# Kernel tuning notes

Hardware: AMD Instinct MI355X
Metric: run time of the kernel (lower is better)

Reference implementation:

```python
import jax, jax.numpy as jnp
import numpy as np
from itertools import permutations

B, S, D = 1024, 16, 128
G_DIMS = [256, 256]
F_DIMS = [256, 256]

# all ordered pairs (i, j), i != j, in the same lexicographic order as
# itertools.permutations used by the torch module
_PAIRS = np.array(list(permutations(range(S), 2)), dtype=np.int32)  # [P, 2], P = S*(S-1)


def _init_linear(key, in_dim, out_dim):
    kw, kb = jax.random.split(key)
    bound = 1.0 / np.sqrt(in_dim)
    W = jax.random.uniform(kw, (in_dim, out_dim), jnp.float32, -bound, bound)
    b = jax.random.uniform(kb, (out_dim,), jnp.float32, -bound, bound)
    return W, b


def setup_inputs() -> dict:
    key = jax.random.key(0)
    ks = jax.random.split(key, 5)
    state = jax.random.normal(ks[0], (B, S, D), jnp.float32)
    gW0, gb0 = _init_linear(ks[1], 2 * D, G_DIMS[0])
    gW1, gb1 = _init_linear(ks[2], G_DIMS[0], G_DIMS[1])
    fW0, fb0 = _init_linear(ks[3], G_DIMS[1], F_DIMS[0])
    fW1, fb1 = _init_linear(ks[4], F_DIMS[0], F_DIMS[1])
    return {"state": state,
            "gW0": gW0, "gb0": gb0, "gW1": gW1, "gb1": gb1,
            "fW0": fW0, "fb0": fb0, "fW1": fW1, "fb1": fb1}


def reference(state, gW0, gb0, gW1, gb1, fW0, fb0, fW1, fb1):
    i_idx = jnp.asarray(_PAIRS[:, 0])
    j_idx = jnp.asarray(_PAIRS[:, 1])
    # gather + concat all ordered pairs: [B, P, 2D]
    paired = jnp.concatenate([state[:, i_idx], state[:, j_idx]], axis=-1)
    # g-MLP applied per pair
    h = jax.nn.relu(jnp.einsum('bpd,de->bpe', paired, gW0) + gb0)
    h = jax.nn.relu(jnp.einsum('bpd,de->bpe', h, gW1) + gb1)
    # sum over pairs -> [B, g_out]
    pooled = h.sum(axis=1)
    # f-MLP
    out = jax.nn.relu(pooled @ fW0 + fb0)
    out = jax.nn.relu(out @ fW1 + fb1)
    return out
```

## Files before the change

### kernel.cpp

```cpp
#include <hip/hip_runtime.h>

typedef __attribute__((ext_vector_type(8))) _Float16 f16x8;
typedef __attribute__((ext_vector_type(4))) float f32x4;

#define HSTR 264

__global__ __launch_bounds__(256) void prep_kernel(
    const float* __restrict__ gW0, const float* __restrict__ gW1,
    _Float16* __restrict__ W0c, _Float16* __restrict__ W1c)
{
  const int t = blockIdx.x * 256 + threadIdx.x;
  {
    const int c = t >> 7, k = t & 127;
    const int dst = ((k >> 5) * 32 + (c >> 4)) * 512 +
                    (((k >> 3) & 3) * 16 + (c & 15)) * 8 + (k & 7);
    const int src = (k + ((c >= 256) ? 128 : 0)) * 256 + (c & 255);
    W0c[dst] = (_Float16)gW0[src];
  }
  {
    const int n = t >> 8, k = t & 255;
    const int dst = ((k >> 5) * 16 + (n >> 4)) * 512 +
                    (((k >> 3) & 3) * 16 + (n & 15)) * 8 + (k & 7);
    W1c[dst] = (_Float16)gW1[k * 256 + n];
  }
}

__global__ __launch_bounds__(512, 4) void pair_kernel(
    const float* __restrict__ state,
    const _Float16* __restrict__ W0c, const float* __restrict__ gb0,
    const _Float16* __restrict__ W1c, const float* __restrict__ gb1,
    float* __restrict__ pooled)
{
  const int b   = blockIdx.x;
  const int tid = threadIdx.x;
  const int w   = tid >> 6;
  const int l   = tid & 63;
  const int lr  = l & 15;
  const int lg  = l >> 4;

  __shared__ _Float16 A_lds[16 * HSTR];
  __shared__ _Float16 C_lds[16 * HSTR];

  const float* stb = state + (size_t)b * 2048;

  f16x8 sfrag[4];
  #pragma unroll
  for (int kk = 0; kk < 4; ++kk) {
    const float* sp = stb + lr * 128 + kk * 32 + lg * 8;
    f32x4 s0 = *(const f32x4*)sp;
    f32x4 s1 = *(const f32x4*)(sp + 4);
    f16x8 f;
    f[0] = (_Float16)s0[0]; f[1] = (_Float16)s0[1];
    f[2] = (_Float16)s0[2]; f[3] = (_Float16)s0[3];
    f[4] = (_Float16)s1[0]; f[5] = (_Float16)s1[1];
    f[6] = (_Float16)s1[2]; f[7] = (_Float16)s1[3];
    sfrag[kk] = f;
  }

  const f32x4 z4 = {0.f, 0.f, 0.f, 0.f};
  f32x4 acc2[4];
  #pragma unroll
  for (int nt = 0; nt < 4; ++nt) acc2[nt] = z4;

  #pragma unroll
  for (int nt = 0; nt < 4; ++nt) {
    #pragma unroll
    for (int kk = 0; kk < 4; ++kk) {
      f16x8 bf = *(const f16x8*)(W0c + (size_t)((kk * 32 + 4 * w + nt) * 512 + l * 8));
      acc2[nt] = __builtin_amdgcn_mfma_f32_16x16x32_f16(sfrag[kk], bf, acc2[nt], 0, 0, 0);
    }
  }

  f16x8 bw[2][8];
  #pragma unroll
  for (int nt = 0; nt < 2; ++nt) {
    #pragma unroll
    for (int kk = 0; kk < 8; ++kk) {
      bw[nt][kk] = *(const f16x8*)(W1c + (size_t)((kk * 16 + 2 * w + nt) * 512 + l * 8));
      asm volatile("" : "+a"(bw[nt][kk]));
    }
  }
  float gb1v[2];
  gb1v[0] = gb1[32 * w + lr];
  gb1v[1] = gb1[32 * w + 16 + lr];

  #pragma unroll
  for (int nt = 0; nt < 4; ++nt) {
    const int col = 64 * w + 16 * nt + lr;
    #pragma unroll
    for (int r = 0; r < 4; ++r) {
      const int row = lg * 4 + r;
      const float v = acc2[nt][r];
      if (col < 256) A_lds[row * HSTR + col]       = (_Float16)(v + gb0[col]);
      else           C_lds[row * HSTR + col - 256] = (_Float16)v;
    }
  }
  __syncthreads();

  f16x8 creg[8];
  #pragma unroll
  for (int kk = 0; kk < 8; ++kk)
    creg[kk] = *(const f16x8*)&C_lds[lr * HSTR + kk * 32 + lg * 8];

  const f16x8 zh = {(_Float16)0, (_Float16)0, (_Float16)0, (_Float16)0,
                    (_Float16)0, (_Float16)0, (_Float16)0, (_Float16)0};

  float pp0 = 0.f, pp1 = 0.f;
  #pragma unroll 1
  for (int i = 0; i < 16; ++i) {
    f32x4 a0 = z4, a1 = z4;
    #pragma unroll
    for (int kk = 0; kk < 8; ++kk) {
      f16x8 av = *(const f16x8*)&A_lds[i * HSTR + kk * 32 + lg * 8];
      f16x8 u = __builtin_elementwise_max(av + creg[kk], zh);
      a0 = __builtin_amdgcn_mfma_f32_16x16x32_f16(u, bw[0][kk], a0, 0, 0, 0);
      a1 = __builtin_amdgcn_mfma_f32_16x16x32_f16(u, bw[1][kk], a1, 0, 0, 0);
    }
    #pragma unroll
    for (int r = 0; r < 4; ++r) {
      const int row = lg * 4 + r;
      const float v0 = fmaxf(a0[r] + gb1v[0], 0.f);
      const float v1 = fmaxf(a1[r] + gb1v[1], 0.f);
      pp0 += (row == i) ? 0.f : v0;
      pp1 += (row == i) ? 0.f : v1;
    }
  }

  {
    float v = pp0;
    v += __shfl_xor(v, 16);
    v += __shfl_xor(v, 32);
    if (lg == 0) pooled[(size_t)b * 256 + 32 * w + lr] = v;
  }
  {
    float v = pp1;
    v += __shfl_xor(v, 16);
    v += __shfl_xor(v, 32);
    if (lg == 0) pooled[(size_t)b * 256 + 32 * w + 16 + lr] = v;
  }
}

__global__ __launch_bounds__(256) void fmlp_kernel(
    const float* __restrict__ pooled,
    const float* __restrict__ fW0, const float* __restrict__ fb0,
    const float* __restrict__ fW1, const float* __restrict__ fb1,
    float* __restrict__ out)
{
  const int tid = threadIdx.x;
  const size_t b0 = (size_t)blockIdx.x * 4;
  __shared__ float pl[4][256];
  __shared__ float h1[4][256];

  #pragma unroll
  for (int q = 0; q < 4; ++q)
    pl[q][tid] = pooled[(b0 + q) * 256 + tid];
  __syncthreads();

  float acc[4] = {0.f, 0.f, 0.f, 0.f};
  #pragma unroll 8
  for (int k = 0; k < 256; ++k) {
    const float wv = fW0[(size_t)k * 256 + tid];
    #pragma unroll
    for (int q = 0; q < 4; ++q) acc[q] = fmaf(pl[q][k], wv, acc[q]);
  }
  #pragma unroll
  for (int q = 0; q < 4; ++q) h1[q][tid] = fmaxf(acc[q] + fb0[tid], 0.f);
  __syncthreads();

  float acc2[4] = {0.f, 0.f, 0.f, 0.f};
  #pragma unroll 8
  for (int k = 0; k < 256; ++k) {
    const float wv = fW1[(size_t)k * 256 + tid];
    #pragma unroll
    for (int q = 0; q < 4; ++q) acc2[q] = fmaf(h1[q][k], wv, acc2[q]);
  }
  #pragma unroll
  for (int q = 0; q < 4; ++q)
    out[(b0 + q) * 256 + tid] = fmaxf(acc2[q] + fb1[tid], 0.f);
}

extern "C" void kernel_launch(void* const* d_in, const int* in_sizes, int n_in,
                              void* d_out, int out_size, void* d_ws, size_t ws_size,
                              hipStream_t stream) {
  const float* state = (const float*)d_in[0];
  const float* gW0   = (const float*)d_in[1];
  const float* gb0   = (const float*)d_in[2];
  const float* gW1   = (const float*)d_in[3];
  const float* gb1   = (const float*)d_in[4];
  const float* fW0   = (const float*)d_in[5];
  const float* fb0   = (const float*)d_in[6];
  const float* fW1   = (const float*)d_in[7];
  const float* fb1   = (const float*)d_in[8];
  float* out = (float*)d_out;

  _Float16* W0c = (_Float16*)d_ws;
  _Float16* W1c = W0c + 65536;
  float* pooled = (float*)(W1c + 65536);

  const int Bn = in_sizes[0] / 2048;

  prep_kernel<<<dim3(256), dim3(256), 0, stream>>>(gW0, gW1, W0c, W1c);
  pair_kernel<<<dim3(Bn), dim3(512), 0, stream>>>(state, W0c, gb0, W1c, gb1, pooled);
  fmlp_kernel<<<dim3(Bn / 4), dim3(256), 0, stream>>>(pooled, fW0, fb0, fW1, fb1, out);
}
```

Measured before the change: 78.13 us.

## Stream W1 fragments from global per iteration and process two pair rows at once

The W1 fragments are no longer held in 16 AGPR-pinned registers for the whole kernel. Each loop iteration now loads them from global/L2, and two i rows are processed per iteration so each loaded fragment feeds two MFMAs. This cuts register pressure, which may allow more waves, and raises MFMA independence. The cost is repeated global weight loads inside the hot loop, eight times per block instead of once.

```diff
diff --git a/kernel.cpp b/kernel.cpp
--- a/kernel.cpp
+++ b/kernel.cpp
@@ -71,15 +71,6 @@
     }
   }
 
-  f16x8 bw[2][8];
-  #pragma unroll
-  for (int nt = 0; nt < 2; ++nt) {
-    #pragma unroll
-    for (int kk = 0; kk < 8; ++kk) {
-      bw[nt][kk] = *(const f16x8*)(W1c + (size_t)((kk * 16 + 2 * w + nt) * 512 + l * 8));
-      asm volatile("" : "+a"(bw[nt][kk]));
-    }
-  }
   float gb1v[2];
   gb1v[0] = gb1[32 * w + lr];
   gb1v[1] = gb1[32 * w + 16 + lr];
@@ -107,22 +98,37 @@
 
   float pp0 = 0.f, pp1 = 0.f;
   #pragma unroll 1
-  for (int i = 0; i < 16; ++i) {
-    f32x4 a0 = z4, a1 = z4;
+  for (int ip = 0; ip < 8; ++ip) {
+    const int i0 = 2 * ip, i1 = 2 * ip + 1;
+    f32x4 a00 = z4, a01 = z4, a10 = z4, a11 = z4;
     #pragma unroll
     for (int kk = 0; kk < 8; ++kk) {
-      f16x8 av = *(const f16x8*)&A_lds[i * HSTR + kk * 32 + lg * 8];
-      f16x8 u = __builtin_elementwise_max(av + creg[kk], zh);
-      a0 = __builtin_amdgcn_mfma_f32_16x16x32_f16(u, bw[0][kk], a0, 0, 0, 0);
-      a1 = __builtin_amdgcn_mfma_f32_16x16x32_f16(u, bw[1][kk], a1, 0, 0, 0);
+      f16x8 av0 = *(const f16x8*)&A_lds[i0 * HSTR + kk * 32 + lg * 8];
+      f16x8 av1 = *(const f16x8*)&A_lds[i1 * HSTR + kk * 32 + lg * 8];
+      f16x8 u0 = __builtin_elementwise_max(av0 + creg[kk], zh);
+      f16x8 u1 = __builtin_elementwise_max(av1 + creg[kk], zh);
+      {
+        f16x8 wf = *(const f16x8*)(W1c + (size_t)((kk * 16 + 2 * w) * 512 + l * 8));
+        a00 = __builtin_amdgcn_mfma_f32_16x16x32_f16(u0, wf, a00, 0, 0, 0);
+        a10 = __builtin_amdgcn_mfma_f32_16x16x32_f16(u1, wf, a10, 0, 0, 0);
+      }
+      {
+        f16x8 wf = *(const f16x8*)(W1c + (size_t)((kk * 16 + 2 * w + 1) * 512 + l * 8));
+        a01 = __builtin_amdgcn_mfma_f32_16x16x32_f16(u0, wf, a01, 0, 0, 0);
+        a11 = __builtin_amdgcn_mfma_f32_16x16x32_f16(u1, wf, a11, 0, 0, 0);
+      }
     }
     #pragma unroll
     for (int r = 0; r < 4; ++r) {
       const int row = lg * 4 + r;
-      const float v0 = fmaxf(a0[r] + gb1v[0], 0.f);
-      const float v1 = fmaxf(a1[r] + gb1v[1], 0.f);
-      pp0 += (row == i) ? 0.f : v0;
-      pp1 += (row == i) ? 0.f : v1;
+      const float v00 = fmaxf(a00[r] + gb1v[0], 0.f);
+      const float v01 = fmaxf(a01[r] + gb1v[1], 0.f);
+      const float v10 = fmaxf(a10[r] + gb1v[0], 0.f);
+      const float v11 = fmaxf(a11[r] + gb1v[1], 0.f);
+      pp0 += (row == i0) ? 0.f : v00;
+      pp1 += (row == i0) ? 0.f : v01;
+      pp0 += (row == i1) ? 0.f : v10;
+      pp1 += (row == i1) ? 0.f : v11;
     }
   }
 
```

Measured after the change: 84.33 us. 7.9% more time.
